# Kernel tuning notes

Hardware: AMD Instinct MI355X
Metric: run time of the kernel (lower is better)

## Reference

```python
import jax, jax.numpy as jnp
import numpy as np
from jax import lax

GRID_SIZE = 3


def setup_inputs() -> dict:
    key = jax.random.key(0)
    k1, k2, k3 = jax.random.split(key, 3)
    B, Cin, Cout, H, W, KH, KW, G = 32, 64, 64, 64, 64, 3, 3, GRID_SIZE
    x = jax.random.normal(k1, (B, Cin, H, W), dtype=jnp.float32)
    scale_base = jax.random.normal(k2, (Cout, Cin, KH, KW), dtype=jnp.float32) * 0.1
    scale_spline = jnp.ones((Cout, Cin, KH, KW), dtype=jnp.float32)
    coeff = jax.random.normal(k3, (2, Cout, Cin, KH, KW, G), dtype=jnp.float32) * 0.02
    bias = jnp.zeros((Cout,), dtype=jnp.float32)
    return {"x": x, "scale_base": scale_base, "scale_spline": scale_spline, "coeff": coeff, "bias": bias}


def _conv(x, w, padding=1):
    return lax.conv_general_dilated(
        x, w, window_strides=(1, 1), padding=((padding, padding), (padding, padding)),
        dimension_numbers=("NCHW", "OIHW", "NCHW"))


def reference(x, scale_base, scale_spline, coeff, bias):
    B, Cin, H, W = x.shape
    Cout, _, KH, KW = scale_base.shape
    G = coeff.shape[-1]
    # Fourier feature expansion: cos(k*x), sin(k*x) for k = 1..G
    ks = jnp.arange(1, G + 1, dtype=x.dtype)
    xk = x[:, :, None] * ks[None, None, :, None, None]          # (B, Cin, G, H, W)
    feats = jnp.concatenate([jnp.cos(xk), jnp.sin(xk)], axis=2)  # (B, Cin, 2G, H, W)
    feats = feats.reshape(B, Cin * 2 * G, H, W)
    # Spline weights: coeff (2, Cout, Cin, KH, KW, G) scaled per-tap -> (Cout, Cin*2G, KH, KW)
    w = coeff * scale_spline[None, :, :, :, :, None]
    w = jnp.transpose(w, (1, 2, 0, 5, 3, 4)).reshape(Cout, Cin * 2 * G, KH, KW)
    # Base branch: SiLU(x) convolved with scale_base
    base = jax.nn.silu(x)
    out = _conv(base, scale_base) + _conv(feats, w)
    out = out + bias[None, :, None, None]
    return out
```

## Files before the change

### kernel.cpp

```cpp
#include <hip/hip_runtime.h>

typedef __attribute__((ext_vector_type(8))) short bf16x8;
typedef __attribute__((ext_vector_type(4))) float f32x4;

#define FROW   4224
#define FBUF4  25344
#define BTRIO  12288
#define LDS_T2 (2 * FBUF4 + 2 * BTRIO)

static __device__ __forceinline__ unsigned short f2bf(float f) {
  union { float f; unsigned u; } v; v.f = f;
  unsigned r = v.u + 0x7fffu + ((v.u >> 16) & 1u);
  return (unsigned short)(r >> 16);
}

static __device__ __forceinline__ void gload16(const void* g, void* l) {
  __builtin_amdgcn_global_load_lds(
      (const __attribute__((address_space(1))) void*)g,
      (__attribute__((address_space(3))) void*)l, 16, 0, 0);
}

__global__ void feats_k(const float* __restrict__ x, const float* __restrict__ sb,
                        const float* __restrict__ ss, const float* __restrict__ cf,
                        unsigned short* __restrict__ fg, unsigned short* __restrict__ wpk) {
  __shared__ __align__(16) unsigned short lds[64 * 456];
  const int b = blockIdx.x, h = blockIdx.y;
  const int tid = threadIdx.x;
  const int w = tid & 63, cig = tid >> 6;
  const int key = ((w + 1) >> 1) & 3;
  const int base = w * 456;
#pragma unroll
  for (int i = 0; i < 16; ++i) {
    int ci = cig * 16 + i;
    float v = x[(((size_t)b * 64 + ci) * 64 + h) * 64 + w];
    float sg = 1.0f / (1.0f + __expf(-v));
    float f0 = v * sg;
    float s1, c1;
    __sincosf(v, &s1, &c1);
    float c2v = c1 * c1 - s1 * s1, s2v = 2.0f * s1 * c1;
    float c3v = c1 * c2v - s1 * s2v, s3v = s1 * c2v + c1 * s2v;
    int q = ci >> 3;
    int half = q >> 2, qq = q & 3;
    int sl = (half * 4 + (qq ^ key)) * 8 + (ci & 7);
    lds[base + 0 * 64 + sl] = f2bf(f0);
    lds[base + 1 * 64 + sl] = f2bf(c1);
    lds[base + 2 * 64 + sl] = f2bf(c2v);
    lds[base + 3 * 64 + sl] = f2bf(c3v);
    lds[base + 4 * 64 + sl] = f2bf(s1);
    lds[base + 5 * 64 + sl] = f2bf(s2v);
    lds[base + 6 * 64 + sl] = f2bf(s3v);
  }
  __syncthreads();
#pragma unroll
  for (int k = 0; k < 14; ++k) {
    int u = tid + k * 256;
    int qs = u & 3;
    int ww = (u >> 2) & 63;
    int c2i = u >> 8;
    int cc = c2i >> 1, half = c2i & 1;
    uint4 v = *(const uint4*)&lds[ww * 456 + cc * 64 + (half * 4 + qs) * 8];
    unsigned short* dst = fg + ((size_t)(c2i * 32 + b) * 64 + h) * 2048 + (ww * 4 + qs) * 8;
    *(uint4*)dst = v;
  }
  if (tid < 126) {
    int idx = (b * 64 + h) * 126 + tid;
    int e = idx & 7;
    int q = (idx >> 3) & 3;
    int co = (idx >> 5) & 63;
    int rest = idx >> 11;
    int tap = rest % 9;
    int c2p = rest / 9;
    int c = c2p >> 1, half = c2p & 1;
    int ci = half * 32 + q * 8 + e;
    int kh = tap / 3, kw = tap % 3;
    int wi = ((co * 64 + ci) * 3 + kh) * 3 + kw;
    float v;
    if (c == 0) {
      v = sb[wi];
    } else {
      int s = (c - 1) / 3, g = (c - 1) % 3;
      v = cf[(s * 36864 + wi) * 3 + g] * ss[wi];
    }
    wpk[((c2p * 9 + tap) * 64 + co) * 32 + ((q ^ ((co >> 1) & 3)) << 3) + e] = f2bf(v);
  }
}

__global__ __launch_bounds__(256, 2) void gemm_k(
    const unsigned short* __restrict__ fg, const unsigned short* __restrict__ wpk,
    const float* __restrict__ bias, float* __restrict__ out) {
  extern __shared__ __align__(16) char smem[];
  const int b = blockIdx.x;
  const int h0 = blockIdx.y * 4;
  const int tid = threadIdx.x;
  const int lane = tid & 63;
  const int wid = tid >> 6;
  const int l15 = lane & 15;
  const int lg = lane >> 4;
  const char* fgB = (const char*)fg;
  const char* wpkB = (const char*)wpk;

  for (int i = tid; i < 2 * FBUF4 / 4; i += 256) {
    int off = i * 4;
    int off2 = (off >= FBUF4) ? off - FBUF4 : off;
    int row = off2 / FROW;
    int cb = off2 - row * FROW;
    int hh = h0 - 1 + row;
    bool staged = ((unsigned)hh < 64u) && (cb >= 64) && (cb < 4160);
    if (!staged) ((int*)smem)[i] = 0;
  }

  int aoff[4][3], boff[4];
#pragma unroll
  for (int cf = 0; cf < 4; ++cf) {
#pragma unroll
    for (int kw = 0; kw < 3; ++kw) {
      int col = cf * 16 + l15 + kw;
      aoff[cf][kw] = col * 64 + ((lg ^ ((col >> 1) & 3)) << 4);
    }
    int co = cf * 16 + l15;
    boff[cf] = co * 64 + ((lg ^ ((co >> 1) & 3)) << 4);
  }

#define STAGE_TRIO(cn, khn, bdst)                                                \
  _Pragma("unroll")                                                              \
  for (int i = 0; i < 3; ++i) {                                                  \
    int u = i * 4 + wid;                        \
    gload16(wpkB + (size_t)((cn) * 9 + (khn) * 3 + (u >> 2)) * 4096 +            \
                (u & 3) * 1024 + lane * 16,                                      \
            (bdst) + (u >> 2) * 4096 + (u & 3) * 1024);                          \
  }
#define STAGE_F8(cn, khp, fdst)                                                  \
  _Pragma("unroll")                                                              \
  for (int j = 0; j < 2; ++j) {                                                  \
    int k = (khp) * 8 + wid * 2 + j;                                  \
    int row = k >> 2, part = k & 3;                                              \
    int hh = h0 - 1 + row;                                                       \
    if ((unsigned)hh < 64u)                                                      \
      gload16(fgB + ((size_t)((cn) * 2048 + b * 64 + hh)) * 4096 +               \
                  part * 1024 + lane * 16,                                       \
              (fdst) + row * FROW + 64 + part * 1024);                           \
  }

#pragma unroll
  for (int p = 0; p < 3; ++p) { STAGE_F8(0, p, smem) }
  STAGE_TRIO(0, 0, smem + 2 * FBUF4)
  __syncthreads();

  f32x4 acc[4][4];
#pragma unroll
  for (int cfi = 0; cfi < 4; ++cfi)
#pragma unroll
    for (int nf = 0; nf < 4; ++nf)
#pragma unroll
      for (int qq = 0; qq < 4; ++qq) acc[cfi][nf][qq] = 0.0f;

  for (int c2 = 0; c2 < 14; ++c2) {
    const char* f = smem + ((c2 & 1) ? FBUF4 : 0);
    char* fnext = smem + (((c2 + 1) & 1) ? FBUF4 : 0);
#pragma unroll
    for (int kh = 0; kh < 3; ++kh) {
      const int khg = c2 * 3 + kh;
      const char* bb = smem + 2 * FBUF4 + ((khg & 1) ? BTRIO : 0);
      if (khg < 41) {
        char* bnext = smem + 2 * FBUF4 + (((khg + 1) & 1) ? BTRIO : 0);
        const int cn = (khg + 1) / 3, khn = (khg + 1) % 3;
        STAGE_TRIO(cn, khn, bnext)
      }
      if (c2 < 13) { STAGE_F8(c2 + 1, kh, fnext) }

      const char* frow = f + (wid + kh) * FROW;
#pragma unroll
      for (int kw = 0; kw < 3; ++kw) {
        bf16x8 A[4], Bv[4];
#pragma unroll
        for (int cfi = 0; cfi < 4; ++cfi)
          A[cfi] = *(const bf16x8*)(frow + aoff[cfi][kw]);
#pragma unroll
        for (int nf = 0; nf < 4; ++nf)
          Bv[nf] = *(const bf16x8*)(bb + kw * 4096 + boff[nf]);
#pragma unroll
        for (int cfi = 0; cfi < 4; ++cfi)
#pragma unroll
          for (int nf = 0; nf < 4; ++nf)
            acc[cfi][nf] = __builtin_amdgcn_mfma_f32_16x16x32_bf16(
                A[cfi], Bv[nf], acc[cfi][nf], 0, 0, 0);
      }
      __syncthreads();
    }
  }
#undef STAGE_TRIO
#undef STAGE_F8

  const int h = h0 + wid;
#pragma unroll
  for (int cfi = 0; cfi < 4; ++cfi) {
    int w4 = cfi * 16 + (lg << 2);
#pragma unroll
    for (int nf = 0; nf < 4; ++nf) {
      int co = nf * 16 + l15;
      float bv = bias[co];
      f32x4 v = acc[cfi][nf];
      f32x4 res;
      res[0] = v[0] + bv; res[1] = v[1] + bv; res[2] = v[2] + bv; res[3] = v[3] + bv;
      *(f32x4*)(out + ((size_t)(b * 64 + co) * 64 + h) * 64 + w4) = res;
    }
  }
}

__global__ void naive_k(const float* __restrict__ x, const float* __restrict__ sb,
                        const float* __restrict__ ss, const float* __restrict__ cf,
                        const float* __restrict__ bias, float* __restrict__ out) {
  int idx = blockIdx.x * 256 + threadIdx.x;
  if (idx >= 32 * 64 * 64 * 64) return;
  int w = idx & 63, h = (idx >> 6) & 63, co = (idx >> 12) & 63, b = idx >> 18;
  float acc = bias[co];
  for (int ci = 0; ci < 64; ++ci) {
    for (int kh = 0; kh < 3; ++kh) {
      int hh = h + kh - 1;
      if ((unsigned)hh >= 64u) continue;
      for (int kw = 0; kw < 3; ++kw) {
        int ww = w + kw - 1;
        if ((unsigned)ww >= 64u) continue;
        float v = x[((b * 64 + ci) * 64 + hh) * 64 + ww];
        int wi = ((co * 64 + ci) * 3 + kh) * 3 + kw;
        float s1, c1; __sincosf(v, &s1, &c1);
        float c2 = c1 * c1 - s1 * s1, s2 = 2.f * s1 * c1;
        float c3 = c1 * c2 - s1 * s2, s3 = s1 * c2 + c1 * s2;
        float t = sb[wi] * (v / (1.f + __expf(-v)));
        t += ss[wi] * (cf[wi * 3] * c1 + cf[wi * 3 + 1] * c2 + cf[wi * 3 + 2] * c3 +
                       cf[(36864 + wi) * 3] * s1 + cf[(36864 + wi) * 3 + 1] * s2 +
                       cf[(36864 + wi) * 3 + 2] * s3);
        acc += t;
      }
    }
  }
  out[idx] = acc;
}

extern "C" void kernel_launch(void* const* d_in, const int* in_sizes, int n_in,
                              void* d_out, int out_size, void* d_ws, size_t ws_size,
                              hipStream_t stream) {
  const float* x = (const float*)d_in[0];
  const float* sb = (const float*)d_in[1];
  const float* ss = (const float*)d_in[2];
  const float* cf = (const float*)d_in[3];
  const float* bias = (const float*)d_in[4];
  float* out = (float*)d_out;

  const size_t FEATS_OFF = 1u << 20;
  const size_t NEED = FEATS_OFF + (size_t)14 * 32 * 64 * 4096;
  if (ws_size >= NEED) {
    unsigned short* wpk = (unsigned short*)d_ws;
    unsigned short* fg = (unsigned short*)((char*)d_ws + FEATS_OFF);
    feats_k<<<dim3(32, 64), 256, 0, stream>>>(x, sb, ss, cf, fg, wpk);
    (void)hipFuncSetAttribute((const void*)gemm_k,
                              hipFuncAttributeMaxDynamicSharedMemorySize, LDS_T2);
    gemm_k<<<dim3(32, 16), 256, LDS_T2, stream>>>(fg, wpk, bias, out);
  } else {
    naive_k<<<32768, 256, 0, stream>>>(x, sb, ss, cf, bias, out);
  }
}
```

Measured before the change: 92.11 us.

## Fuse Fourier/SiLU feature generation into the GEMM kernel, dropping the feature buffer

Removes the separate feature-materialisation kernel, which wrote a large bf16 feature tensor to global memory that the GEMM then read back. Each GEMM block now computes the SiLU/cos/sin features for its rows directly from x and writes them into the LDS double buffer. Weight packing moves into its own small kernel. This saves global traffic and a kernel, but adds transcendental math and strided x loads, with halo rows recomputed by neighbouring blocks, inside the GEMM pipeline where they may stall the MFMA loop.

```diff
diff --git a/kernel.cpp b/kernel.cpp
--- a/kernel.cpp
+++ b/kernel.cpp
@@ -20,73 +20,32 @@
       (__attribute__((address_space(3))) void*)l, 16, 0, 0);
 }
 
-__global__ void feats_k(const float* __restrict__ x, const float* __restrict__ sb,
-                        const float* __restrict__ ss, const float* __restrict__ cf,
-                        unsigned short* __restrict__ fg, unsigned short* __restrict__ wpk) {
-  __shared__ __align__(16) unsigned short lds[64 * 456];
-  const int b = blockIdx.x, h = blockIdx.y;
-  const int tid = threadIdx.x;
-  const int w = tid & 63, cig = tid >> 6;
-  const int key = ((w + 1) >> 1) & 3;
-  const int base = w * 456;
-#pragma unroll
-  for (int i = 0; i < 16; ++i) {
-    int ci = cig * 16 + i;
-    float v = x[(((size_t)b * 64 + ci) * 64 + h) * 64 + w];
-    float sg = 1.0f / (1.0f + __expf(-v));
-    float f0 = v * sg;
-    float s1, c1;
-    __sincosf(v, &s1, &c1);
-    float c2v = c1 * c1 - s1 * s1, s2v = 2.0f * s1 * c1;
-    float c3v = c1 * c2v - s1 * s2v, s3v = s1 * c2v + c1 * s2v;
-    int q = ci >> 3;
-    int half = q >> 2, qq = q & 3;
-    int sl = (half * 4 + (qq ^ key)) * 8 + (ci & 7);
-    lds[base + 0 * 64 + sl] = f2bf(f0);
-    lds[base + 1 * 64 + sl] = f2bf(c1);
-    lds[base + 2 * 64 + sl] = f2bf(c2v);
-    lds[base + 3 * 64 + sl] = f2bf(c3v);
-    lds[base + 4 * 64 + sl] = f2bf(s1);
-    lds[base + 5 * 64 + sl] = f2bf(s2v);
-    lds[base + 6 * 64 + sl] = f2bf(s3v);
-  }
-  __syncthreads();
-#pragma unroll
-  for (int k = 0; k < 14; ++k) {
-    int u = tid + k * 256;
-    int qs = u & 3;
-    int ww = (u >> 2) & 63;
-    int c2i = u >> 8;
-    int cc = c2i >> 1, half = c2i & 1;
-    uint4 v = *(const uint4*)&lds[ww * 456 + cc * 64 + (half * 4 + qs) * 8];
-    unsigned short* dst = fg + ((size_t)(c2i * 32 + b) * 64 + h) * 2048 + (ww * 4 + qs) * 8;
-    *(uint4*)dst = v;
-  }
-  if (tid < 126) {
-    int idx = (b * 64 + h) * 126 + tid;
-    int e = idx & 7;
-    int q = (idx >> 3) & 3;
-    int co = (idx >> 5) & 63;
-    int rest = idx >> 11;
-    int tap = rest % 9;
-    int c2p = rest / 9;
-    int c = c2p >> 1, half = c2p & 1;
-    int ci = half * 32 + q * 8 + e;
-    int kh = tap / 3, kw = tap % 3;
-    int wi = ((co * 64 + ci) * 3 + kh) * 3 + kw;
-    float v;
-    if (c == 0) {
-      v = sb[wi];
-    } else {
-      int s = (c - 1) / 3, g = (c - 1) % 3;
-      v = cf[(s * 36864 + wi) * 3 + g] * ss[wi];
-    }
-    wpk[((c2p * 9 + tap) * 64 + co) * 32 + ((q ^ ((co >> 1) & 3)) << 3) + e] = f2bf(v);
-  }
+__global__ void pack_w_k(const float* __restrict__ sb, const float* __restrict__ ss,
+                         const float* __restrict__ cf, unsigned short* __restrict__ wpk) {
+  int idx = blockIdx.x * 256 + threadIdx.x;
+  if (idx >= 126 * 64 * 32) return;
+  int e = idx & 7;
+  int q = (idx >> 3) & 3;
+  int co = (idx >> 5) & 63;
+  int rest = idx >> 11;
+  int tap = rest % 9;
+  int c2 = rest / 9;
+  int c = c2 >> 1, half = c2 & 1;
+  int ci = half * 32 + q * 8 + e;
+  int kh = tap / 3, kw = tap % 3;
+  int wi = ((co * 64 + ci) * 3 + kh) * 3 + kw;
+  float v;
+  if (c == 0) {
+    v = sb[wi];
+  } else {
+    int s = (c - 1) / 3, g = (c - 1) % 3;
+    v = cf[(s * 36864 + wi) * 3 + g] * ss[wi];
+  }
+  wpk[((c2 * 9 + tap) * 64 + co) * 32 + ((q ^ ((co >> 1) & 3)) << 3) + e] = f2bf(v);
 }
 
 __global__ __launch_bounds__(256, 2) void gemm_k(
-    const unsigned short* __restrict__ fg, const unsigned short* __restrict__ wpk,
+    const float* __restrict__ x, const unsigned short* __restrict__ wpk,
     const float* __restrict__ bias, float* __restrict__ out) {
   extern __shared__ __align__(16) char smem[];
   const int b = blockIdx.x;
@@ -96,8 +55,12 @@
   const int wid = tid >> 6;
   const int l15 = lane & 15;
   const int lg = lane >> 4;
-  const char* fgB = (const char*)fg;
   const char* wpkB = (const char*)wpk;
+
+  const int fw = tid & 63;
+  const int fq = tid >> 6;
+  const int fcol = fw + 1;
+  const int fsl16 = (fq ^ ((fcol >> 1) & 3)) << 4;
 
   for (int i = tid; i < 2 * FBUF4 / 4; i += 256) {
     int off = i * 4;
@@ -124,25 +87,42 @@
 #define STAGE_TRIO(cn, khn, bdst)                                                \
   _Pragma("unroll")                                                              \
   for (int i = 0; i < 3; ++i) {                                                  \
-    int u = i * 4 + wid;                        \
+    int u = i * 4 + wid;                                                         \
     gload16(wpkB + (size_t)((cn) * 9 + (khn) * 3 + (u >> 2)) * 4096 +            \
                 (u & 3) * 1024 + lane * 16,                                      \
             (bdst) + (u >> 2) * 4096 + (u & 3) * 1024);                          \
   }
-#define STAGE_F8(cn, khp, fdst)                                                  \
-  _Pragma("unroll")                                                              \
-  for (int j = 0; j < 2; ++j) {                                                  \
-    int k = (khp) * 8 + wid * 2 + j;                                  \
-    int row = k >> 2, part = k & 3;                                              \
-    int hh = h0 - 1 + row;                                                       \
-    if ((unsigned)hh < 64u)                                                      \
-      gload16(fgB + ((size_t)((cn) * 2048 + b * 64 + hh)) * 4096 +               \
-                  part * 1024 + lane * 16,                                       \
-              (fdst) + row * FROW + 64 + part * 1024);                           \
-  }
-
-#pragma unroll
-  for (int p = 0; p < 3; ++p) { STAGE_F8(0, p, smem) }
+
+#define FEATGEN_P(cn, p, fdst)                                                   \
+  {                                                                              \
+    const int c_ = (cn) >> 1, half_ = (cn) & 1;                                  \
+    const float* xq_ = x + ((size_t)(b * 64 + half_ * 32 + fq * 8) * 64) * 64 + fw; \
+    _Pragma("unroll")                                                            \
+    for (int rr = 0; rr < 2; ++rr) {                                             \
+      int r = (p) * 2 + rr;                                                      \
+      int hh = h0 - 1 + r;                                                       \
+      if ((unsigned)hh < 64u) {                                                  \
+        bf16x8 pk;                                                               \
+        _Pragma("unroll")                                                        \
+        for (int e = 0; e < 8; ++e) {                                            \
+          float v = xq_[(size_t)e * 4096 + hh * 64];                             \
+          float val;                                                             \
+          if (c_ == 0)      val = v / (1.0f + __expf(-v));                       \
+          else if (c_ == 1) val = __cosf(v);                                     \
+          else if (c_ == 2) val = __cosf(2.0f * v);                              \
+          else if (c_ == 3) val = __cosf(3.0f * v);                              \
+          else if (c_ == 4) val = __sinf(v);                                     \
+          else if (c_ == 5) val = __sinf(2.0f * v);                              \
+          else              val = __sinf(3.0f * v);                              \
+          pk[e] = (short)f2bf(val);                                              \
+        }                                                                        \
+        *(bf16x8*)((fdst) + r * FROW + fcol * 64 + fsl16) = pk;                  \
+      }                                                                          \
+    }                                                                            \
+  }
+
+#pragma unroll
+  for (int p = 0; p < 3; ++p) { FEATGEN_P(0, p, smem) }
   STAGE_TRIO(0, 0, smem + 2 * FBUF4)
   __syncthreads();
 
@@ -166,7 +146,7 @@
         const int cn = (khg + 1) / 3, khn = (khg + 1) % 3;
         STAGE_TRIO(cn, khn, bnext)
       }
-      if (c2 < 13) { STAGE_F8(c2 + 1, kh, fnext) }
+      if (c2 < 13) { FEATGEN_P(c2 + 1, kh, fnext) }
 
       const char* frow = f + (wid + kh) * FROW;
 #pragma unroll
@@ -189,7 +169,7 @@
     }
   }
 #undef STAGE_TRIO
-#undef STAGE_F8
+#undef FEATGEN_P
 
   const int h = h0 + wid;
 #pragma unroll
@@ -247,15 +227,13 @@
   const float* bias = (const float*)d_in[4];
   float* out = (float*)d_out;
 
-  const size_t FEATS_OFF = 1u << 20;
-  const size_t NEED = FEATS_OFF + (size_t)14 * 32 * 64 * 4096;
+  const size_t NEED = 1u << 20;
   if (ws_size >= NEED) {
     unsigned short* wpk = (unsigned short*)d_ws;
-    unsigned short* fg = (unsigned short*)((char*)d_ws + FEATS_OFF);
-    feats_k<<<dim3(32, 64), 256, 0, stream>>>(x, sb, ss, cf, fg, wpk);
+    pack_w_k<<<1008, 256, 0, stream>>>(sb, ss, cf, wpk);
     (void)hipFuncSetAttribute((const void*)gemm_k,
                               hipFuncAttributeMaxDynamicSharedMemorySize, LDS_T2);
-    gemm_k<<<dim3(32, 16), 256, LDS_T2, stream>>>(fg, wpk, bias, out);
+    gemm_k<<<dim3(32, 16), 256, LDS_T2, stream>>>(x, wpk, bias, out);
   } else {
     naive_k<<<32768, 256, 0, stream>>>(x, sb, ss, cf, bias, out);
   }
```

Result: slower. 233.8 us (+153.8%).
